# Optimization experiments

Hardware: AMD Instinct MI355X
Metric: run time of the kernel (lower is better)

Reference implementation:

```python
import jax, jax.numpy as jnp
import numpy as np

B, N, C, H = 8, 1024, 1024, 16
DH = C // H
SCALE = DH ** -0.5
EPS = 1e-6


def layernorm(x, g, b):
    m = jnp.mean(x, axis=-1, keepdims=True)
    v = jnp.mean(jnp.square(x - m), axis=-1, keepdims=True)
    return (x - m) * jax.lax.rsqrt(v + EPS) * g + b


def setup_inputs() -> dict:
    key = jax.random.key(0)
    ks = jax.random.split(key, 5)
    w = 0.02  # init std for weights, keeps activations sane
    return {
        "x": jax.random.normal(ks[0], (B, N, C), jnp.float32),
        "qkv_w": jax.random.normal(ks[1], (C, 3 * C), jnp.float32) * w,
        "qkv_b": jnp.zeros((3 * C,), jnp.float32),
        "proj_w": jax.random.normal(ks[2], (C, C), jnp.float32) * w,
        "proj_b": jnp.zeros((C,), jnp.float32),
        "n1_g": jnp.ones((C,), jnp.float32),
        "n1_b": jnp.zeros((C,), jnp.float32),
        "fc1_w": jax.random.normal(ks[3], (C, 4 * C), jnp.float32) * w,
        "fc1_b": jnp.zeros((4 * C,), jnp.float32),
        "fc2_w": jax.random.normal(ks[4], (4 * C, C), jnp.float32) * w,
        "fc2_b": jnp.zeros((C,), jnp.float32),
        "n2_g": jnp.ones((C,), jnp.float32),
        "n2_b": jnp.zeros((C,), jnp.float32),
    }


def reference(x, qkv_w, qkv_b, proj_w, proj_b, n1_g, n1_b,
              fc1_w, fc1_b, fc2_w, fc2_b, n2_g, n2_b):
    # --- manual multi-head attention (timm-style, materializes BxHxNxN) ---
    qkv = x @ qkv_w + qkv_b                                  # [B,N,3C]
    qkv = qkv.reshape(B, N, 3, H, DH).transpose(2, 0, 3, 1, 4)  # [3,B,H,N,DH]
    q, k, v = qkv[0], qkv[1], qkv[2]
    attn = jax.nn.softmax(jnp.einsum('bhnd,bhmd->bhnm', q, k) * SCALE, axis=-1)
    y = jnp.einsum('bhnm,bhmd->bhnd', attn, v)               # [B,H,N,DH]
    y = y.transpose(0, 2, 1, 3).reshape(B, N, C)
    y = y @ proj_w + proj_b                                  # attention output replaces x
    # --- NOTE: unusual block wiring, faithful to source ---
    # x = attn_out; x = x + norm1(x); x = x + norm2(mlp(x))
    y = y + layernorm(y, n1_g, n1_b)
    h = jax.nn.gelu(y @ fc1_w + fc1_b, approximate=False)    # timm Mlp: fc1 -> GELU -> fc2
    h = h @ fc2_w + fc2_b
    y = y + layernorm(h, n2_g, n2_b)
    return y
```

## Files before the change

kernel.cpp:

```cpp
#include <hip/hip_runtime.h>
#include <hip/hip_bf16.h>
#include <math.h>

typedef __bf16 bf16;
typedef __bf16 bf16x8 __attribute__((ext_vector_type(8)));
typedef float f32x4 __attribute__((ext_vector_type(4)));

__device__ __forceinline__ int swz_idx(int row, int col) {
    return ((row) << 6) + (((((col) >> 3) ^ ((row) & 7)) << 3) | ((col) & 7));
}
#define LDS_SWZ8(row, c8) ((((row)) << 6) + ((((c8) ^ ((row) & 7))) << 3))

__device__ __forceinline__ void gload_lds16(const bf16* g, bf16* l) {
    __builtin_amdgcn_global_load_lds(
        (const __attribute__((address_space(1))) void*)g,
        (__attribute__((address_space(3))) void*)l,
        16, 0, 0);
}

template <int ROWS>
__device__ __forceinline__ void stage_swz(const bf16* __restrict__ src, long rstride,
                                          bf16* lds, int tid) {
#pragma unroll
    for (int pass = 0; pass < ROWS / 32; ++pass) {
        int e = pass * 2048 + tid * 8;
        int r = e >> 6;
        int c8 = (e >> 3) & 7;
        int sc8 = c8 ^ (r & 7);
        gload_lds16(src + (long)r * rstride + sc8 * 8, lds + e);
    }
}

__device__ __forceinline__ float bf2f(unsigned short u) {
    unsigned int v = (unsigned int)u << 16;
    return __builtin_bit_cast(float, v);
}
__device__ __forceinline__ short f2bf_s(float f) {
    return (short)__builtin_bit_cast(unsigned short, (bf16)f);
}

__global__ __launch_bounds__(256)
void preprocess_all(const float* __restrict__ qkv_w, const float* __restrict__ proj_w,
                    const float* __restrict__ fc1_w, const float* __restrict__ fc2_w,
                    const float* __restrict__ x,
                    bf16* __restrict__ qkvT, bf16* __restrict__ projT,
                    bf16* __restrict__ fc1T, bf16* __restrict__ fc2T,
                    bf16* __restrict__ xbf) {
    const int id = blockIdx.x;
    const int tid = threadIdx.x;

    if (id >= 12288) {
        long i = ((long)(id - 12288) * 256 + tid) * 4;
        float4 v = *(const float4*)(x + i);
        short4 pk;
        pk.x = f2bf_s(v.x); pk.y = f2bf_s(v.y); pk.z = f2bf_s(v.z); pk.w = f2bf_s(v.w);
        *(short4*)(xbf + i) = pk;
        return;
    }

    const float* src; bf16* dst; int R, C, bx, by;
    if (id < 3072)      { src = qkv_w; dst = qkvT; R = 1024; C = 3072; bx = id % 96;  by = id / 96; }
    else if (id < 4096) { int t = id - 3072; src = proj_w; dst = projT; R = 1024; C = 1024; bx = t % 32;  by = t / 32; }
    else if (id < 8192) { int t = id - 4096; src = fc1_w;  dst = fc1T;  R = 1024; C = 4096; bx = t % 128; by = t / 128; }
    else                { int t = id - 8192; src = fc2_w;  dst = fc2T;  R = 4096; C = 1024; bx = t % 32;  by = t / 32; }

    __shared__ float tile[32][33];
    const int tx = tid & 31, ty = tid >> 5;
#pragma unroll
    for (int j = 0; j < 32; j += 8)
        tile[ty + j][tx] = src[(long)(by * 32 + ty + j) * C + bx * 32 + tx];
    __syncthreads();
#pragma unroll
    for (int j = 0; j < 32; j += 8)
        dst[(long)(bx * 32 + ty + j) * R + by * 32 + tx] = (bf16)tile[tx][ty + j];
}

template <int MODE>
__global__ __launch_bounds__(256, 4)
void gemm_bt(const bf16* __restrict__ A, const bf16* __restrict__ Bt,
             const float* __restrict__ bias,
             float* __restrict__ Cf, bf16* __restrict__ Cb0,
             bf16* __restrict__ Cb1, bf16* __restrict__ Cb2,
             int M, int N, int K) {
    __shared__ __align__(16) bf16 lsA[128 * 64];
    __shared__ __align__(16) bf16 lsB[128 * 64];

    const int nwg = gridDim.x * gridDim.y;
    const int lin = blockIdx.y * gridDim.x + blockIdx.x;
    const int swz = (lin & 7) * (nwg >> 3) + (lin >> 3);
    const int bx = swz % gridDim.x, by = swz / gridDim.x;

    const int tid = threadIdx.x;
    const int lane = tid & 63;
    const int w = tid >> 6;
    const int wm = w >> 1, wn = w & 1;
    const int l15 = lane & 15, l4 = lane >> 4;
    const int row0 = by * 128;
    const int col0 = bx * 128;

    f32x4 acc[4][4] = {};

    for (int k0 = 0; k0 < K; k0 += 64) {
        stage_swz<128>(A + (long)row0 * K + k0, K, lsA, tid);
        stage_swz<128>(Bt + (long)col0 * K + k0, K, lsB, tid);
        __syncthreads();
#pragma unroll
        for (int kk = 0; kk < 2; ++kk) {
            int c8 = kk * 4 + l4;
            bf16x8 af[4], bfr[4];
#pragma unroll
            for (int mt = 0; mt < 4; ++mt)
                af[mt] = *(const bf16x8*)(&lsA[LDS_SWZ8(wm * 64 + mt * 16 + l15, c8)]);
#pragma unroll
            for (int nt = 0; nt < 4; ++nt)
                bfr[nt] = *(const bf16x8*)(&lsB[LDS_SWZ8(wn * 64 + nt * 16 + l15, c8)]);
#pragma unroll
            for (int mt = 0; mt < 4; ++mt)
#pragma unroll
                for (int nt = 0; nt < 4; ++nt)
                    acc[mt][nt] = __builtin_amdgcn_mfma_f32_16x16x32_bf16(
                        af[mt], bfr[nt], acc[mt][nt], 0, 0, 0);
        }
        __syncthreads();
    }

#pragma unroll
    for (int mt = 0; mt < 4; ++mt) {
#pragma unroll
        for (int nt = 0; nt < 4; ++nt) {
            int colb = col0 + wn * 64 + nt * 16 + l15;
            float bv = bias[colb];
#pragma unroll
            for (int i = 0; i < 4; ++i) {
                int row = row0 + wm * 64 + mt * 16 + l4 * 4 + i;
                int col = colb;
                float v = acc[mt][nt][i] + bv;
                if (MODE == 0) {
                    int b = row >> 10, nn = row & 1023;
                    int s = col >> 10, rem = col & 1023;
                    int h = rem >> 6, d = rem & 63;
                    long bh = (long)b * 16 + h;
                    if (s == 0)      Cb0[(bh * 1024 + nn) * 64 + d] = (bf16)(v * 0.1803368881f);
                    else if (s == 1) Cb1[(bh * 1024 + nn) * 64 + d] = (bf16)v;
                    else             Cb2[(bh * 64 + d) * 1024 + nn] = (bf16)v;
                } else if (MODE == 1) {
                    Cb0[(long)row * N + col] = (bf16)v;
                } else if (MODE == 2) {
                    float g = 0.5f * v * (1.0f + erff(v * 0.70710678118f));
                    Cb0[(long)row * N + col] = (bf16)g;
                } else {
                    Cf[(long)row * N + col] = v;
                }
            }
        }
    }
}

__global__ __launch_bounds__(256, 4)
void attn_flash(const bf16* __restrict__ Q, const bf16* __restrict__ Kv,
                const bf16* __restrict__ Vt, bf16* __restrict__ Y) {
    __shared__ __align__(16) bf16 lsK[2][64 * 64];
    __shared__ __align__(16) bf16 lsV[2][64 * 64];
    __shared__ __align__(16) bf16 lsP[4][16 * 64];

    const int raw = blockIdx.x;
    const int c   = raw & 7;
    const int g   = raw >> 3;
    const int bh  = c * 16 + (g >> 4);
    const int q0  = (g & 15) * 64;

    const int tid = threadIdx.x;
    const int lane = tid & 63;
    const int w = tid >> 6;
    const int l15 = lane & 15, l4 = lane >> 4;
    const int b = bh >> 4, h = bh & 15;

    const bf16* qp = Q + ((long)bh * 1024 + q0 + w * 16 + l15) * 64;
    bf16x8 qa[2];
    qa[0] = *(const bf16x8*)(qp + 8 * l4);
    qa[1] = *(const bf16x8*)(qp + 32 + 8 * l4);

    const bf16* kbase = Kv + (long)bh * 1024 * 64;
    const bf16* vbase = Vt + (long)bh * 64 * 1024;

    float lsum[4] = {0.f, 0.f, 0.f, 0.f};
    f32x4 oacc[4] = {};

    stage_swz<64>(kbase, 64, lsK[0], tid);
    stage_swz<64>(vbase, 1024, lsV[0], tid);
    __syncthreads();

    for (int t = 0; t < 16; ++t) {
        const int cur = t & 1;
        if (t < 15) {
            int kv0 = (t + 1) * 64;
            stage_swz<64>(kbase + (long)kv0 * 64, 64, lsK[cur ^ 1], tid);
            stage_swz<64>(vbase + kv0, 1024, lsV[cur ^ 1], tid);
        }

        f32x4 s[4] = {};
        __builtin_amdgcn_s_setprio(1);
#pragma unroll
        for (int kk = 0; kk < 2; ++kk) {
            int c8 = kk * 4 + l4;
#pragma unroll
            for (int nt = 0; nt < 4; ++nt) {
                bf16x8 kb = *(const bf16x8*)(&lsK[cur][LDS_SWZ8(nt * 16 + l15, c8)]);
                s[nt] = __builtin_amdgcn_mfma_f32_16x16x32_bf16(qa[kk], kb, s[nt], 0, 0, 0);
            }
        }
        __builtin_amdgcn_s_setprio(0);

#pragma unroll
        for (int i = 0; i < 4; ++i) {
            int prow = l4 * 4 + i;
#pragma unroll
            for (int nt = 0; nt < 4; ++nt) {
                float p = exp2f(s[nt][i]);
                lsum[i] += p;
                lsP[w][swz_idx(prow, nt * 16 + l15)] = (bf16)p;
            }
        }
        __builtin_amdgcn_sched_barrier(0);
        asm volatile("s_waitcnt lgkmcnt(0)" ::: "memory");
        __builtin_amdgcn_sched_barrier(0);

        __builtin_amdgcn_s_setprio(1);
#pragma unroll
        for (int kk = 0; kk < 2; ++kk) {
            int c8 = kk * 4 + l4;
            bf16x8 pa = *(const bf16x8*)(&lsP[w][LDS_SWZ8(l15, c8)]);
#pragma unroll
            for (int nt = 0; nt < 4; ++nt) {
                bf16x8 vb = *(const bf16x8*)(&lsV[cur][LDS_SWZ8(nt * 16 + l15, c8)]);
                oacc[nt] = __builtin_amdgcn_mfma_f32_16x16x32_bf16(pa, vb, oacc[nt], 0, 0, 0);
            }
        }
        __builtin_amdgcn_s_setprio(0);
        __syncthreads();
    }

#pragma unroll
    for (int i = 0; i < 4; ++i) {
#pragma unroll
        for (int off = 1; off < 16; off <<= 1)
            lsum[i] += __shfl_xor(lsum[i], off);
    }

#pragma unroll
    for (int i = 0; i < 4; ++i) {
        float rinv = 1.0f / lsum[i];
        int row = q0 + w * 16 + l4 * 4 + i;
#pragma unroll
        for (int nt = 0; nt < 4; ++nt) {
            int d = nt * 16 + l15;
            Y[((long)b * 1024 + row) * 1024 + h * 64 + d] = (bf16)(oacc[nt][i] * rinv);
        }
    }
}

__device__ __forceinline__ float block_reduce_sum(float v, float* sm) {
#pragma unroll
    for (int off = 1; off < 64; off <<= 1) v += __shfl_xor(v, off);
    int w = threadIdx.x >> 6;
    if ((threadIdx.x & 63) == 0) sm[w] = v;
    __syncthreads();
    v = sm[0] + sm[1] + sm[2] + sm[3];
    __syncthreads();
    return v;
}

__global__ __launch_bounds__(256)
void res_ln(const bf16* __restrict__ Yin, bf16* __restrict__ Yout,
            const float* __restrict__ g, const float* __restrict__ beta) {
    __shared__ float sm[4];
    const long row = blockIdx.x;
    const int t = threadIdx.x;
    short4 raw = *(const short4*)(Yin + row * 1024 + t * 4);
    float x0 = bf2f((unsigned short)raw.x), x1 = bf2f((unsigned short)raw.y);
    float x2 = bf2f((unsigned short)raw.z), x3 = bf2f((unsigned short)raw.w);
    float s = x0 + x1 + x2 + x3;
    s = block_reduce_sum(s, sm);
    float mean = s * (1.0f / 1024.0f);
    float d0 = x0 - mean, d1 = x1 - mean, d2 = x2 - mean, d3 = x3 - mean;
    float sq = d0 * d0 + d1 * d1 + d2 * d2 + d3 * d3;
    sq = block_reduce_sum(sq, sm);
    float rs = rsqrtf(sq * (1.0f / 1024.0f) + 1e-6f);
    float4 gg = *(const float4*)(g + t * 4);
    float4 bb = *(const float4*)(beta + t * 4);
    short4 pk;
    pk.x = f2bf_s(x0 + d0 * rs * gg.x + bb.x);
    pk.y = f2bf_s(x1 + d1 * rs * gg.y + bb.y);
    pk.z = f2bf_s(x2 + d2 * rs * gg.z + bb.z);
    pk.w = f2bf_s(x3 + d3 * rs * gg.w + bb.w);
    *(short4*)(Yout + row * 1024 + t * 4) = pk;
}

__global__ __launch_bounds__(256)
void final_ln(float* __restrict__ Hf, const bf16* __restrict__ Yres,
              const float* __restrict__ g, const float* __restrict__ beta) {
    __shared__ float sm[4];
    const long row = blockIdx.x;
    float* p = Hf + row * 1024;
    const int t = threadIdx.x;
    float4 x = *(const float4*)(p + t * 4);
    float s = x.x + x.y + x.z + x.w;
    s = block_reduce_sum(s, sm);
    float mean = s * (1.0f / 1024.0f);
    float d0 = x.x - mean, d1 = x.y - mean, d2 = x.z - mean, d3 = x.w - mean;
    float sq = d0 * d0 + d1 * d1 + d2 * d2 + d3 * d3;
    sq = block_reduce_sum(sq, sm);
    float rs = rsqrtf(sq * (1.0f / 1024.0f) + 1e-6f);
    float4 gg = *(const float4*)(g + t * 4);
    float4 bb = *(const float4*)(beta + t * 4);
    short4 yr = *(const short4*)(Yres + row * 1024 + t * 4);
    float4 o;
    o.x = bf2f((unsigned short)yr.x) + d0 * rs * gg.x + bb.x;
    o.y = bf2f((unsigned short)yr.y) + d1 * rs * gg.y + bb.y;
    o.z = bf2f((unsigned short)yr.z) + d2 * rs * gg.z + bb.z;
    o.w = bf2f((unsigned short)yr.w) + d3 * rs * gg.w + bb.w;
    *(float4*)(p + t * 4) = o;
}

extern "C" void kernel_launch(void* const* d_in, const int* in_sizes, int n_in,
                              void* d_out, int out_size, void* d_ws, size_t ws_size,
                              hipStream_t stream) {
    const float* x      = (const float*)d_in[0];
    const float* qkv_w  = (const float*)d_in[1];
    const float* qkv_b  = (const float*)d_in[2];
    const float* proj_w = (const float*)d_in[3];
    const float* proj_b = (const float*)d_in[4];
    const float* n1_g   = (const float*)d_in[5];
    const float* n1_b   = (const float*)d_in[6];
    const float* fc1_w  = (const float*)d_in[7];
    const float* fc1_b  = (const float*)d_in[8];
    const float* fc2_w  = (const float*)d_in[9];
    const float* fc2_b  = (const float*)d_in[10];
    const float* n2_g   = (const float*)d_in[11];
    const float* n2_b   = (const float*)d_in[12];

    char* ws = (char*)d_ws;
    const long MB = 1l << 20;
    bf16*  qkvT   = (bf16*)(ws + 0 * MB);
    bf16*  projT  = (bf16*)(ws + 6 * MB);
    bf16*  fc1T   = (bf16*)(ws + 8 * MB);
    bf16*  fc2T   = (bf16*)(ws + 16 * MB);
    bf16*  xbf    = (bf16*)(ws + 24 * MB);
    bf16*  yattn  = (bf16*)(ws + 24 * MB);
    bf16*  qb     = (bf16*)(ws + 40 * MB);
    bf16*  kb     = (bf16*)(ws + 56 * MB);
    bf16*  vtb    = (bf16*)(ws + 72 * MB);
    bf16*  yprojb = (bf16*)(ws + 40 * MB);
    bf16*  yresb  = (bf16*)(ws + 72 * MB);
    bf16*  h1     = (bf16*)(ws + 88 * MB);
    float* outf   = (float*)d_out;

    preprocess_all<<<20480, 256, 0, stream>>>(qkv_w, proj_w, fc1_w, fc2_w, x,
                                              qkvT, projT, fc1T, fc2T, xbf);

    gemm_bt<0><<<dim3(3072 / 128, 8192 / 128), 256, 0, stream>>>(
        xbf, qkvT, qkv_b, nullptr, qb, kb, vtb, 8192, 3072, 1024);
    attn_flash<<<2048, 256, 0, stream>>>(qb, kb, vtb, yattn);
    gemm_bt<1><<<dim3(1024 / 128, 8192 / 128), 256, 0, stream>>>(
        yattn, projT, proj_b, nullptr, yprojb, nullptr, nullptr, 8192, 1024, 1024);
    res_ln<<<8192, 256, 0, stream>>>(yprojb, yresb, n1_g, n1_b);
    gemm_bt<2><<<dim3(4096 / 128, 8192 / 128), 256, 0, stream>>>(
        yresb, fc1T, fc1_b, nullptr, h1, nullptr, nullptr, 8192, 4096, 1024);
    gemm_bt<3><<<dim3(1024 / 128, 8192 / 128), 256, 0, stream>>>(
        h1, fc2T, fc2_b, outf, nullptr, nullptr, nullptr, 8192, 1024, 4096);
    final_ln<<<8192, 256, 0, stream>>>(outf, yresb, n2_g, n2_b);
}
```

Baseline: 358.5 us.

## Precompute GEMM LDS offsets, widen attention blocks to 512 threads, bf16 fc2 output

The GEMM hoists its swizzled LDS read offsets and global staging offsets out of the k-loop. The attention kernel now runs 512-thread blocks over 128 query rows, each thread staging one 16-byte chunk of K and V per tile. The fc2 GEMM writes bf16 into the workspace instead of fp32, and the final layernorm reads it and writes fp32 to the output, cutting intermediate traffic. The risks are lower occupancy from the 512-thread launch bounds and extra rounding of the fc2 output before the final layernorm.

```diff
diff --git a/kernel.cpp b/kernel.cpp
--- a/kernel.cpp
+++ b/kernel.cpp
@@ -16,19 +16,6 @@
         (const __attribute__((address_space(1))) void*)g,
         (__attribute__((address_space(3))) void*)l,
         16, 0, 0);
-}
-
-template <int ROWS>
-__device__ __forceinline__ void stage_swz(const bf16* __restrict__ src, long rstride,
-                                          bf16* lds, int tid) {
-#pragma unroll
-    for (int pass = 0; pass < ROWS / 32; ++pass) {
-        int e = pass * 2048 + tid * 8;
-        int r = e >> 6;
-        int c8 = (e >> 3) & 7;
-        int sc8 = c8 ^ (r & 7);
-        gload_lds16(src + (long)r * rstride + sc8 * 8, lds + e);
-    }
 }
 
 __device__ __forceinline__ float bf2f(unsigned short u) {
@@ -98,22 +85,43 @@
     const int row0 = by * 128;
     const int col0 = bx * 128;
 
+    int aofs[2][4], bofs[2][4];
+#pragma unroll
+    for (int kk = 0; kk < 2; ++kk) {
+#pragma unroll
+        for (int t = 0; t < 4; ++t) {
+            aofs[kk][t] = LDS_SWZ8(wm * 64 + t * 16 + l15, kk * 4 + l4);
+            bofs[kk][t] = LDS_SWZ8(wn * 64 + t * 16 + l15, kk * 4 + l4);
+        }
+    }
+    const bf16* baseA = A + (long)row0 * K;
+    const bf16* baseB = Bt + (long)col0 * K;
+    const int sr = tid >> 3;
+    const int sc8 = (tid & 7) ^ (sr & 7);
+    int voff[4];
+#pragma unroll
+    for (int p = 0; p < 4; ++p) voff[p] = (p * 32 + sr) * K + sc8 * 8;
+    const int ldst = tid * 8;
+
     f32x4 acc[4][4] = {};
 
     for (int k0 = 0; k0 < K; k0 += 64) {
-        stage_swz<128>(A + (long)row0 * K + k0, K, lsA, tid);
-        stage_swz<128>(Bt + (long)col0 * K + k0, K, lsB, tid);
+#pragma unroll
+        for (int p = 0; p < 4; ++p)
+            gload_lds16(baseA + k0 + voff[p], lsA + p * 2048 + ldst);
+#pragma unroll
+        for (int p = 0; p < 4; ++p)
+            gload_lds16(baseB + k0 + voff[p], lsB + p * 2048 + ldst);
         __syncthreads();
 #pragma unroll
         for (int kk = 0; kk < 2; ++kk) {
-            int c8 = kk * 4 + l4;
             bf16x8 af[4], bfr[4];
 #pragma unroll
             for (int mt = 0; mt < 4; ++mt)
-                af[mt] = *(const bf16x8*)(&lsA[LDS_SWZ8(wm * 64 + mt * 16 + l15, c8)]);
+                af[mt] = *(const bf16x8*)(lsA + aofs[kk][mt]);
 #pragma unroll
             for (int nt = 0; nt < 4; ++nt)
-                bfr[nt] = *(const bf16x8*)(&lsB[LDS_SWZ8(wn * 64 + nt * 16 + l15, c8)]);
+                bfr[nt] = *(const bf16x8*)(lsB + bofs[kk][nt]);
 #pragma unroll
             for (int mt = 0; mt < 4; ++mt)
 #pragma unroll
@@ -156,18 +164,18 @@
     }
 }
 
-__global__ __launch_bounds__(256, 4)
+__global__ __launch_bounds__(512, 2)
 void attn_flash(const bf16* __restrict__ Q, const bf16* __restrict__ Kv,
                 const bf16* __restrict__ Vt, bf16* __restrict__ Y) {
     __shared__ __align__(16) bf16 lsK[2][64 * 64];
     __shared__ __align__(16) bf16 lsV[2][64 * 64];
-    __shared__ __align__(16) bf16 lsP[4][16 * 64];
+    __shared__ __align__(16) bf16 lsP[8][16 * 64];
 
     const int raw = blockIdx.x;
     const int c   = raw & 7;
     const int g   = raw >> 3;
-    const int bh  = c * 16 + (g >> 4);
-    const int q0  = (g & 15) * 64;
+    const int bh  = c * 16 + (g >> 3);
+    const int q0  = (g & 7) * 128;
 
     const int tid = threadIdx.x;
     const int lane = tid & 63;
@@ -183,19 +191,24 @@
     const bf16* kbase = Kv + (long)bh * 1024 * 64;
     const bf16* vbase = Vt + (long)bh * 64 * 1024;
 
+    const int sr = tid >> 3;
+    const int sc8 = (tid & 7) ^ (sr & 7);
+    const int kvoff = sr * 64 + sc8 * 8;
+    const int vvoff = sr * 1024 + sc8 * 8;
+    const int ldst = tid * 8;
+
     float lsum[4] = {0.f, 0.f, 0.f, 0.f};
     f32x4 oacc[4] = {};
 
-    stage_swz<64>(kbase, 64, lsK[0], tid);
-    stage_swz<64>(vbase, 1024, lsV[0], tid);
+    gload_lds16(kbase + kvoff, lsK[0] + ldst);
+    gload_lds16(vbase + vvoff, lsV[0] + ldst);
     __syncthreads();
 
     for (int t = 0; t < 16; ++t) {
         const int cur = t & 1;
         if (t < 15) {
-            int kv0 = (t + 1) * 64;
-            stage_swz<64>(kbase + (long)kv0 * 64, 64, lsK[cur ^ 1], tid);
-            stage_swz<64>(vbase + kv0, 1024, lsV[cur ^ 1], tid);
+            gload_lds16(kbase + (t + 1) * 4096 + kvoff, lsK[cur ^ 1] + ldst);
+            gload_lds16(vbase + (t + 1) * 64 + vvoff, lsV[cur ^ 1] + ldst);
         }
 
         f32x4 s[4] = {};
@@ -297,17 +310,19 @@
 }
 
 __global__ __launch_bounds__(256)
-void final_ln(float* __restrict__ Hf, const bf16* __restrict__ Yres,
+void final_ln(const bf16* __restrict__ Hb, const bf16* __restrict__ Yres,
+              float* __restrict__ Out,
               const float* __restrict__ g, const float* __restrict__ beta) {
     __shared__ float sm[4];
     const long row = blockIdx.x;
-    float* p = Hf + row * 1024;
     const int t = threadIdx.x;
-    float4 x = *(const float4*)(p + t * 4);
-    float s = x.x + x.y + x.z + x.w;
+    short4 hr = *(const short4*)(Hb + row * 1024 + t * 4);
+    float x0 = bf2f((unsigned short)hr.x), x1 = bf2f((unsigned short)hr.y);
+    float x2 = bf2f((unsigned short)hr.z), x3 = bf2f((unsigned short)hr.w);
+    float s = x0 + x1 + x2 + x3;
     s = block_reduce_sum(s, sm);
     float mean = s * (1.0f / 1024.0f);
-    float d0 = x.x - mean, d1 = x.y - mean, d2 = x.z - mean, d3 = x.w - mean;
+    float d0 = x0 - mean, d1 = x1 - mean, d2 = x2 - mean, d3 = x3 - mean;
     float sq = d0 * d0 + d1 * d1 + d2 * d2 + d3 * d3;
     sq = block_reduce_sum(sq, sm);
     float rs = rsqrtf(sq * (1.0f / 1024.0f) + 1e-6f);
@@ -319,7 +334,7 @@
     o.y = bf2f((unsigned short)yr.y) + d1 * rs * gg.y + bb.y;
     o.z = bf2f((unsigned short)yr.z) + d2 * rs * gg.z + bb.z;
     o.w = bf2f((unsigned short)yr.w) + d3 * rs * gg.w + bb.w;
-    *(float4*)(p + t * 4) = o;
+    *(float4*)(Out + row * 1024 + t * 4) = o;
 }
 
 extern "C" void kernel_launch(void* const* d_in, const int* in_sizes, int n_in,
@@ -352,6 +367,7 @@
     bf16*  vtb    = (bf16*)(ws + 72 * MB);
     bf16*  yprojb = (bf16*)(ws + 40 * MB);
     bf16*  yresb  = (bf16*)(ws + 72 * MB);
+    bf16*  hb     = (bf16*)(ws + 40 * MB);
     bf16*  h1     = (bf16*)(ws + 88 * MB);
     float* outf   = (float*)d_out;
 
@@ -360,13 +376,13 @@
 
     gemm_bt<0><<<dim3(3072 / 128, 8192 / 128), 256, 0, stream>>>(
         xbf, qkvT, qkv_b, nullptr, qb, kb, vtb, 8192, 3072, 1024);
-    attn_flash<<<2048, 256, 0, stream>>>(qb, kb, vtb, yattn);
+    attn_flash<<<1024, 512, 0, stream>>>(qb, kb, vtb, yattn);
     gemm_bt<1><<<dim3(1024 / 128, 8192 / 128), 256, 0, stream>>>(
         yattn, projT, proj_b, nullptr, yprojb, nullptr, nullptr, 8192, 1024, 1024);
     res_ln<<<8192, 256, 0, stream>>>(yprojb, yresb, n1_g, n1_b);
     gemm_bt<2><<<dim3(4096 / 128, 8192 / 128), 256, 0, stream>>>(
         yresb, fc1T, fc1_b, nullptr, h1, nullptr, nullptr, 8192, 4096, 1024);
-    gemm_bt<3><<<dim3(1024 / 128, 8192 / 128), 256, 0, stream>>>(
-        h1, fc2T, fc2_b, outf, nullptr, nullptr, nullptr, 8192, 1024, 4096);
-    final_ln<<<8192, 256, 0, stream>>>(outf, yresb, n2_g, n2_b);
-}
+    gemm_bt<1><<<dim3(1024 / 128, 8192 / 128), 256, 0, stream>>>(
+        h1, fc2T, fc2_b, nullptr, hb, nullptr, nullptr, 8192, 1024, 4096);
+    final_ln<<<8192, 256, 0, stream>>>(hb, yresb, outf, n2_g, n2_b);
+}
```

After: 351.4 us, median of 3. 2.0% less time.
